# Performance work log

Hardware: AMD Instinct MI355X
Metric: run time of the kernel (lower is better)

## Reference

```python
import math
import jax, jax.numpy as jnp
import numpy as np

B, S, D, H = 2, 2048, 1024, 16


def setup_inputs() -> dict:
    key = jax.random.key(0)
    ks = jax.random.split(key, 8)
    scale = 1.0 / math.sqrt(D)
    kv_mask = jax.random.randint(ks[1], (B, S), 0, 2).astype(bool)
    kv_mask = kv_mask.at[:, 0].set(True)  # ensure at least one valid kv per batch
    return {
        "q": jax.random.normal(ks[0], (B, S, D), dtype=jnp.float32),
        "kv_mask": kv_mask,
        "Wq": jax.random.normal(ks[2], (D, D), dtype=jnp.float32) * scale,
        "Wk": jax.random.normal(ks[3], (D, D), dtype=jnp.float32) * scale,
        "Wv": jax.random.normal(ks[4], (D, D), dtype=jnp.float32) * scale,
        "Wo": jax.random.normal(ks[5], (D, D), dtype=jnp.float32) * scale,
        "bo": jax.random.normal(ks[6], (D,), dtype=jnp.float32) * 0.01,
        "num_heads": H,
    }


def _pass_with_mask(x, W, mask, b=None):
    # Linear applied everywhere, output zeroed where mask is False (pass_with_mask)
    y = x @ W.T
    if b is not None:
        y = y + b
    return jnp.where(mask[..., None], y, 0.0)


def reference(q, kv_mask, Wq, Wk, Wv, Wo, bo, num_heads):
    b, s, d = q.shape
    hd = d // num_heads
    q_mask = jnp.ones((b, s), dtype=bool)  # default q_mask in the module
    # self-attention: k = v = q
    qh = _pass_with_mask(q, Wq, q_mask).reshape(b, s, num_heads, hd)
    kh = _pass_with_mask(q, Wk, kv_mask).reshape(b, s, num_heads, hd)
    vh = _pass_with_mask(q, Wv, kv_mask).reshape(b, s, num_heads, hd)
    # scores: note the module scales by sqrt(model_dim), NOT sqrt(head_dim)
    scores = jnp.einsum("bqhd,bkhd->bhqk", qh, kh) / math.sqrt(d)
    mask = (q_mask[:, :, None] & kv_mask[:, None, :])[:, None, :, :]  # [b,1,q,k]
    scores = jnp.where(mask, scores, -jnp.inf)
    attn = jax.nn.softmax(scores, axis=-1)
    attn = jnp.where(mask, attn, 0.0)
    out = jnp.einsum("bhqk,bkhd->bqhd", attn, vh).reshape(b, s, d)
    return _pass_with_mask(out, Wo, q_mask, bo)
```

## Files before the change

kernel.cpp:

```cpp
#include <hip/hip_runtime.h>
#include <math.h>

#define B_ 2
#define S_ 2048
#define DM 1024
#define NH 16
#define HD 64

typedef unsigned short u16;
typedef unsigned int u32;
typedef __attribute__((ext_vector_type(8))) short bf16x8;
typedef __attribute__((ext_vector_type(4))) float f32x4;

#define C2SCALE 0.0450842200277800f

__device__ __forceinline__ u16 f2bf(float x) {
  unsigned u = __float_as_uint(x);
  u = (u + 0x7FFFu + ((u >> 16) & 1u)) >> 16;
  return (u16)u;
}

__device__ __forceinline__ u32 cvtpk(float lo, float hi) {
  u32 r;
  asm("v_cvt_pk_bf16_f32 %0, %1, %2" : "=v"(r) : "v"(lo), "v"(hi));
  return r;
}

__device__ __forceinline__ float exp2a(float x) {
  float r;
  asm("v_exp_f32 %0, %1" : "=v"(r) : "v"(x));
  return r;
}

__device__ __forceinline__ void gload_lds16(const u16* g, u16* l) {
  __builtin_amdgcn_global_load_lds((const __attribute__((address_space(1))) void*)g,
                                   (__attribute__((address_space(3))) void*)l, 16, 0, 0);
}

__device__ __forceinline__ int sigpos(int w6) {
  return ((w6 >> 5) << 5) | (((w6 >> 2) & 3) << 3) | (((w6 >> 4) & 1) << 2) | (w6 & 3);
}

__global__ void mask_scan(const int* __restrict__ kvm, int* __restrict__ posb,
                          int* __restrict__ nvb, u16* __restrict__ mwg) {
  const int b = blockIdx.x;
  const int tid = threadIdx.x;
  const int lane = tid & 63, wv = tid >> 6;
  __shared__ int wsum[4];
  int v[8], s = 0;
  const int base = b * S_ + tid * 8;
#pragma unroll
  for (int j = 0; j < 8; j++) { v[j] = kvm[base + j] ? 1 : 0; s += v[j]; }
  int sc = s;
#pragma unroll
  for (int off = 1; off < 64; off <<= 1) {
    int t = __shfl_up(sc, off, 64);
    if (lane >= off) sc += t;
  }
  if (lane == 63) wsum[wv] = sc;
  __syncthreads();
  int woff = 0;
#pragma unroll
  for (int w = 0; w < 4; w++) woff += (w < wv) ? wsum[w] : 0;
  int run = woff + sc - s;
#pragma unroll
  for (int j = 0; j < 8; j++) { posb[base + j] = run; run += v[j]; }
  const int total = wsum[0] + wsum[1] + wsum[2] + wsum[3];
  if (tid == 0) nvb[b] = total;
  for (int i = tid; i < S_; i += 256)
    mwg[b * S_ + (i & ~63) + sigpos(i & 63)] = (i < total) ? 0xFFFFu : 0u;
}

__global__ void cvt_all(const float* __restrict__ q, const float* __restrict__ Wq,
                        const float* __restrict__ Wk, const float* __restrict__ Wv,
                        const float* __restrict__ Wo, const int* __restrict__ kvm,
                        const int* __restrict__ posb, const int* __restrict__ nvb,
                        u16* __restrict__ Xbf, u16* __restrict__ Wcat,
                        u16* __restrict__ Wobf, u16* __restrict__ vtbuf,
                        u16* __restrict__ Xc) {
  const int NQ4 = (B_ * S_ * DM) / 4;
  const int NW4 = (DM * DM) / 4;
  const int total = NQ4 + 4 * NW4;
  int i = blockIdx.x * blockDim.x + threadIdx.x;
  int stride = gridDim.x * blockDim.x;
  for (int idx = i; idx < B_ * NH * HD * 64; idx += stride) {
    int col = idx & 63;
    int dd = (idx >> 6) & 63;
    int bh = idx >> 12;
    int nv = nvb[bh >> 4];
    int padw = ((nv + 63) & ~63) - nv;
    if (col < padw)
      vtbuf[((size_t)bh * HD + dd) * S_ + nv + col] = 0;
  }
  for (; i < total; i += stride) {
    if (i < NQ4) {
      float4 v = ((const float4*)q)[i];
      ushort4 o;
      o.x = f2bf(v.x); o.y = f2bf(v.y); o.z = f2bf(v.z); o.w = f2bf(v.w);
      ((ushort4*)Xbf)[i] = o;
      int row = i >> 8, chunk = i & 255;
      int b = row >> 11, s = row & 2047;
      if (kvm[b * S_ + s]) {
        int p = posb[b * S_ + s];
        *(ushort4*)(Xc + ((size_t)(b * S_ + p)) * DM + chunk * 4) = o;
      }
    } else {
      int t = i - NQ4;
      const float* src;
      u16* dst;
      if (t < NW4)            { src = Wq + (size_t)t * 4; dst = Wcat + (size_t)t * 4; }
      else if (t < 2 * NW4)   { src = Wk + (size_t)(t - NW4) * 4;     dst = Wcat + DM * DM + (size_t)(t - NW4) * 4; }
      else if (t < 3 * NW4)   { src = Wv + (size_t)(t - 2 * NW4) * 4; dst = Wcat + 2 * DM * DM + (size_t)(t - 2 * NW4) * 4; }
      else                    { src = Wo + (size_t)(t - 3 * NW4) * 4; dst = Wobf + (size_t)(t - 3 * NW4) * 4; }
      float4 v = *(const float4*)src;
      ushort4 o;
      o.x = f2bf(v.x); o.y = f2bf(v.y); o.z = f2bf(v.z); o.w = f2bf(v.w);
      *(ushort4*)dst = o;
    }
  }
}

__global__ __launch_bounds__(512, 6) void gemm_qkv(
    const u16* __restrict__ Xbf, const u16* __restrict__ Xc,
    const u16* __restrict__ Wcat, u16* __restrict__ qo, u16* __restrict__ ko,
    u16* __restrict__ vo, const int* __restrict__ nvb) {
  const int K = DM;
  const int Lraw = blockIdx.x;
  const int Ls = (Lraw & 7) * 96 + (Lraw >> 3);

  int Mb, nglob, bkv = 0, nv = 1 << 30;
  const u16* Ap;
  if (Ls < 256) {
    Mb = (Ls & 31) << 7;
    nglob = (Ls >> 5) << 7;
    Ap = Xbf;
  } else {
    int L2 = Ls - 256;
    bkv = L2 >> 8;
    int L3 = L2 & 255;
    Mb = (L3 & 15) << 7;
    nglob = 1024 + ((L3 >> 4) << 7);
    nv = nvb[bkv];
    if (Mb >= nv) return;
    Ap = Xc + (size_t)bkv * S_ * DM;
  }

  __shared__ __align__(16) u16 As[2][64 * 64];
  __shared__ __align__(16) u16 Bs[2][64 * 64];
  const int tid = threadIdx.x;
  const int wv = tid >> 6, lane = tid & 63;
  const int g = lane >> 4, c = lane & 15;
  const int wr = wv >> 1, wc = wv & 1;

  f32x4 acc[2][4];
#pragma unroll
  for (int i = 0; i < 2; i++)
#pragma unroll
    for (int j = 0; j < 4; j++) acc[i][j] = f32x4{0.f, 0.f, 0.f, 0.f};

  const int srow = tid >> 3;
  const int scol8 = tid & 7;
  const int m1 = srow * 2 + (scol8 >> 2);
  const int kkc = (scol8 & 3) * 8;
  const u16* ag = Ap + (size_t)(Mb + m1) * K + kkc;
  const u16* bg = Wcat + (size_t)(nglob + m1) * K + kkc;
  const int slot = scol8 ^ (srow & 7);
  u16* al = &As[0][srow * 64 + slot * 8];
  u16* bl = &Bs[0][srow * 64 + slot * 8];

  bf16x8 ar = *(const bf16x8*)ag;
  bf16x8 br = *(const bf16x8*)bg;
  *(bf16x8*)al = ar;
  *(bf16x8*)bl = br;
  ar = *(const bf16x8*)(ag + 32);
  br = *(const bf16x8*)(bg + 32);
  __syncthreads();

  const int off = ((((c & 1) << 2) | g) ^ (c >> 1)) << 3;
  const int arb = (wr * 16 + (c >> 1)) * 64 + off;
  const int brb = (wc * 32 + (c >> 1)) * 64 + off;

  for (int t = 0; t < 32; ++t) {
    const int cur = t & 1;
    if (t + 1 < 32) {
      const int nb = (cur ^ 1) * 4096;
      *(bf16x8*)(al + nb) = ar;
      *(bf16x8*)(bl + nb) = br;
      if (t + 2 < 32) {
        ar = *(const bf16x8*)(ag + (t + 2) * 32);
        br = *(const bf16x8*)(bg + (t + 2) * 32);
      }
    }
    const u16* AB = &As[cur][0];
    const u16* BB = &Bs[cur][0];
    bf16x8 af[2], bfr[4];
#pragma unroll
    for (int mi = 0; mi < 2; mi++)
      af[mi] = *(const bf16x8*)&AB[arb + mi * 512];
#pragma unroll
    for (int ni = 0; ni < 4; ni++)
      bfr[ni] = *(const bf16x8*)&BB[brb + ni * 512];
#pragma unroll
    for (int mi = 0; mi < 2; mi++)
#pragma unroll
      for (int ni = 0; ni < 4; ni++)
        acc[mi][ni] = __builtin_amdgcn_mfma_f32_16x16x32_bf16(af[mi], bfr[ni], acc[mi][ni], 0, 0, 0);
    asm volatile("s_waitcnt lgkmcnt(0)\n\ts_barrier" ::: "memory");
  }

  const int nbase = nglob + wc * 64 + c;
  const int which = nbase >> 10;
  if (which == 0) {
#pragma unroll
    for (int mi = 0; mi < 2; mi++) {
#pragma unroll
      for (int ni = 0; ni < 4; ni++) {
        int nn = nbase + ni * 16;
        int h = nn >> 6, d = nn & 63;
#pragma unroll
        for (int r = 0; r < 4; r++) {
          int row = Mb + wr * 32 + mi * 16 + g * 4 + r;
          int b0 = row >> 11, s0 = row & 2047;
          qo[(((size_t)(b0 * NH + h)) * S_ + s0) * HD + d] =
              f2bf(acc[mi][ni][r] * C2SCALE);
        }
      }
    }
  } else if (which == 1) {
#pragma unroll
    for (int mi = 0; mi < 2; mi++) {
#pragma unroll
      for (int r = 0; r < 4; r++) {
        int p = Mb + wr * 32 + mi * 16 + g * 4 + r;
        if (p < nv) {
#pragma unroll
          for (int ni = 0; ni < 4; ni++) {
            int nn = (nbase + ni * 16) & 1023;
            ko[((size_t)(bkv * NH + (nn >> 6)) * S_ + p) * HD + (nn & 63)] =
                f2bf(acc[mi][ni][r]);
          }
        }
      }
    }
  } else {
#pragma unroll
    for (int mi = 0; mi < 2; mi++) {
#pragma unroll
      for (int r = 0; r < 4; r++) {
        int p = Mb + wr * 32 + mi * 16 + g * 4 + r;
        if (p < nv) {
          int dst = (p & ~63) + sigpos(p & 63);
#pragma unroll
          for (int ni = 0; ni < 4; ni++) {
            int nn = (nbase + ni * 16) & 1023;
            vo[((size_t)((bkv * NH + (nn >> 6)) * HD + (nn & 63))) * S_ + dst] =
                f2bf(acc[mi][ni][r]);
          }
        }
      }
    }
  }
}

__global__ __launch_bounds__(256, 4) void gemm_n64(
    const u16* __restrict__ A, const u16* __restrict__ Bw,
    const float* __restrict__ bias, float* __restrict__ fo) {
  __shared__ __align__(16) u16 As[128 * 32];
  __shared__ __align__(16) u16 Bs[64 * 32];
  const int K = DM, N = DM;
  const int tid = threadIdx.x;
  const int wv = tid >> 6, lane = tid & 63;
  const int g = lane >> 4, c = lane & 15;
  const int wr = wv >> 1, wc = wv & 1;
  const int L = blockIdx.x;
  const int Ls = (L & 7) * 64 + (L >> 3);
  const int Mb = (Ls & 31) << 7, Nb = (Ls >> 5) << 6;

  f32x4 acc[4][2];
#pragma unroll
  for (int i = 0; i < 4; i++)
#pragma unroll
    for (int j = 0; j < 2; j++) acc[i][j] = f32x4{0.f, 0.f, 0.f, 0.f};

  for (int kb = 0; kb < K; kb += 32) {
#pragma unroll
    for (int it = 0; it < 2; ++it) {
      int id = it * 256 + tid;
      int m = id >> 2, kk = (id & 3) * 8;
      gload_lds16(A + (size_t)(Mb + m) * K + kb + kk, As + (it * 4 + wv) * 512);
    }
    {
      int m = tid >> 2, kk = (tid & 3) * 8;
      gload_lds16(Bw + (size_t)(Nb + m) * K + kb + kk, Bs + wv * 512);
    }
    __syncthreads();
    bf16x8 af[4], bfr[2];
#pragma unroll
    for (int mi = 0; mi < 4; mi++)
      af[mi] = *(const bf16x8*)(As + (wr * 64 + mi * 16 + c) * 32 + g * 8);
#pragma unroll
    for (int ni = 0; ni < 2; ni++)
      bfr[ni] = *(const bf16x8*)(Bs + (wc * 32 + ni * 16 + c) * 32 + g * 8);
#pragma unroll
    for (int mi = 0; mi < 4; mi++)
#pragma unroll
      for (int ni = 0; ni < 2; ni++)
        acc[mi][ni] = __builtin_amdgcn_mfma_f32_16x16x32_bf16(af[mi], bfr[ni], acc[mi][ni], 0, 0, 0);
    __syncthreads();
  }

#pragma unroll
  for (int mi = 0; mi < 4; mi++) {
#pragma unroll
    for (int ni = 0; ni < 2; ni++) {
      int n = Nb + wc * 32 + ni * 16 + c;
      float bv = bias[n];
#pragma unroll
      for (int r = 0; r < 4; r++) {
        int row = Mb + wr * 64 + mi * 16 + g * 4 + r;
        fo[(size_t)row * N + n] = acc[mi][ni][r] + bv;
      }
    }
  }
}

__global__ __launch_bounds__(512, 4) void attn_kernel(
    const u16* __restrict__ qb, const u16* __restrict__ kb,
    const u16* __restrict__ vtb, const u16* __restrict__ mwg,
    const int* __restrict__ nvb, u16* __restrict__ ob) {
  __shared__ __align__(16) u16 Kl[2][64 * 64];
  __shared__ __align__(16) u16 Vl[2][64 * 64];
  __shared__ __align__(16) u16 MW[S_];

  const int tid = threadIdx.x;
  const int wv = tid >> 6, lane = tid & 63;
  const int g = lane >> 4, c = lane & 15;

  const int L = blockIdx.x;
  const int j = L >> 3;
  const int bh = ((L & 7) << 2) | (j >> 4);
  const int qi = j & 15;
  const int b = bh >> 4, h = bh & 15;
  const int q0 = qi * 128;
  const size_t bhbase = (size_t)bh * (S_ * HD);
  const int NT = (nvb[b] + 63) >> 6;

  ((uint2*)MW)[tid] = ((const uint2*)(mwg + b * S_))[tid];

  bf16x8 qf[2];
#pragma unroll
  for (int ks = 0; ks < 2; ks++)
    qf[ks] = *(const bf16x8*)(qb + bhbase + (size_t)(q0 + wv * 16 + c) * HD + ks * 32 + g * 8);

  f32x4 Oa[4];
#pragma unroll
  for (int di = 0; di < 4; di++) Oa[di] = f32x4{0.f, 0.f, 0.f, 0.f};
  f32x4 lacc = f32x4{0.f, 0.f, 0.f, 0.f};

  union { u32 u[4]; bf16x8 v; } ones;
#pragma unroll
  for (int w = 0; w < 4; w++) ones.u[w] = 0x3F803F80u;

  const int srow = tid >> 3;
  const int scol8 = tid & 7;
  const u16* kg = kb + bhbase + (size_t)srow * HD + scol8 * 8;
  const u16* vg = vtb + bhbase + (size_t)srow * S_ + scol8 * 8;
  const int wslot = scol8 ^ (srow & 7);
  u16* kld = &Kl[0][srow * 64 + wslot * 8];
  u16* vld = &Vl[0][srow * 64 + wslot * 8];

  bf16x8 krg = *(const bf16x8*)kg;
  bf16x8 vrg = *(const bf16x8*)vg;
  *(bf16x8*)kld = krg;
  *(bf16x8*)vld = vrg;
  krg = *(const bf16x8*)(kg + 64 * HD);
  vrg = *(const bf16x8*)(vg + 64);
  __syncthreads();

  const int swz = c & 7;

  for (int t = 0; t < NT; ++t) {
    const int cur = t & 1;
    if (t + 1 < NT) {
      *(bf16x8*)(kld + (cur ^ 1) * 4096) = krg;
      *(bf16x8*)(vld + (cur ^ 1) * 4096) = vrg;
      if (t + 2 < NT) {
        krg = *(const bf16x8*)(kg + (t + 2) * (64 * HD));
        vrg = *(const bf16x8*)(vg + (t + 2) * 64);
      }
    }
    const u16* KB = &Kl[cur][0];
    const u16* VB = &Vl[cur][0];

    f32x4 Sa[4];
#pragma unroll
    for (int ni = 0; ni < 4; ni++) Sa[ni] = f32x4{0.f, 0.f, 0.f, 0.f};
    __builtin_amdgcn_s_setprio(1);
#pragma unroll
    for (int ks = 0; ks < 2; ks++) {
      bf16x8 kf[4];
#pragma unroll
      for (int ni = 0; ni < 4; ni++)
        kf[ni] = *(const bf16x8*)&KB[(ni * 16 + c) * 64 + (((4 * ks + g) ^ swz) * 8)];
#pragma unroll
      for (int ni = 0; ni < 4; ni++)
        Sa[ni] = __builtin_amdgcn_mfma_f32_16x16x32_bf16(kf[ni], qf[ks], Sa[ni], 0, 0, 0);
    }
    __builtin_amdgcn_s_setprio(0);

    bf16x8 Pa[2];
#pragma unroll
    for (int ks = 0; ks < 2; ks++) {
      uint4 mw = *(const uint4*)&MW[t * 64 + ks * 32 + g * 8];
      union { u32 u[4]; bf16x8 v; } pw;
      pw.u[0] = cvtpk(exp2a(Sa[2 * ks][0]), exp2a(Sa[2 * ks][1])) & mw.x;
      pw.u[1] = cvtpk(exp2a(Sa[2 * ks][2]), exp2a(Sa[2 * ks][3])) & mw.y;
      pw.u[2] = cvtpk(exp2a(Sa[2 * ks + 1][0]), exp2a(Sa[2 * ks + 1][1])) & mw.z;
      pw.u[3] = cvtpk(exp2a(Sa[2 * ks + 1][2]), exp2a(Sa[2 * ks + 1][3])) & mw.w;
      Pa[ks] = pw.v;
    }

    __builtin_amdgcn_s_setprio(1);
    lacc = __builtin_amdgcn_mfma_f32_16x16x32_bf16(ones.v, Pa[0], lacc, 0, 0, 0);
    lacc = __builtin_amdgcn_mfma_f32_16x16x32_bf16(ones.v, Pa[1], lacc, 0, 0, 0);
#pragma unroll
    for (int ks = 0; ks < 2; ks++) {
      bf16x8 vf[4];
#pragma unroll
      for (int di = 0; di < 4; di++)
        vf[di] = *(const bf16x8*)&VB[(di * 16 + c) * 64 + (((4 * ks + g) ^ swz) * 8)];
#pragma unroll
      for (int di = 0; di < 4; di++)
        Oa[di] = __builtin_amdgcn_mfma_f32_16x16x32_bf16(vf[di], Pa[ks], Oa[di], 0, 0, 0);
    }
    __builtin_amdgcn_s_setprio(0);

    asm volatile("s_waitcnt lgkmcnt(0)\n\ts_barrier" ::: "memory");
  }

  float inv = 1.f / lacc[0];
  int q = q0 + wv * 16 + c;
  size_t base = ((size_t)(b * S_ + q)) * DM + (size_t)h * HD;
#pragma unroll
  for (int di = 0; di < 4; di++) {
    uint2 o;
    o.x = cvtpk(Oa[di][0] * inv, Oa[di][1] * inv);
    o.y = cvtpk(Oa[di][2] * inv, Oa[di][3] * inv);
    *(uint2*)(ob + base + di * 16 + g * 4) = o;
  }
}

extern "C" void kernel_launch(void* const* d_in, const int* in_sizes, int n_in,
                              void* d_out, int out_size, void* d_ws, size_t ws_size,
                              hipStream_t stream) {
  const float* q  = (const float*)d_in[0];
  const int* kvm  = (const int*)d_in[1];
  const float* Wq = (const float*)d_in[2];
  const float* Wk = (const float*)d_in[3];
  const float* Wv = (const float*)d_in[4];
  const float* Wo = (const float*)d_in[5];
  const float* bo = (const float*)d_in[6];
  float* out = (float*)d_out;
  char* ws = (char*)d_ws;

  u16* Xbf   = (u16*)(ws);
  u16* Wcat  = (u16*)(ws + (8u << 20));
  u16* Wobf  = (u16*)(ws + (14u << 20));
  u16* qbuf  = (u16*)(ws + (16u << 20));
  u16* kbuf  = (u16*)(ws + (24u << 20));
  u16* vtbuf = (u16*)(ws + (32u << 20));
  u16* mwg   = (u16*)(ws + (40u << 20));
  int* posb  = (int*)(ws + (41u << 20));
  int* nvb   = (int*)(ws + (42u << 20));
  u16* Xc    = (u16*)d_out;
  u16* obuf  = Xbf;

  mask_scan<<<B_, 256, 0, stream>>>(kvm, posb, nvb, mwg);
  cvt_all<<<2048, 256, 0, stream>>>(q, Wq, Wk, Wv, Wo, kvm, posb, nvb,
                                    Xbf, Wcat, Wobf, vtbuf, Xc);
  gemm_qkv<<<768, 512, 0, stream>>>(Xbf, Xc, Wcat, qbuf, kbuf, vtbuf, nvb);
  attn_kernel<<<512, 512, 0, stream>>>(qbuf, kbuf, vtbuf, mwg, nvb, obuf);
  gemm_n64<<<512, 256, 0, stream>>>(obuf, Wobf, bo, out);
}
```

Before: 110.3 us.

## Give each attention wave two 16-row query tiles and halve the block size

The attention kernel now launches 256 threads per block (4 waves), and each wave handles 32 query rows as two 16-row MFMA tiles instead of 16 rows. Every K/V fragment read from shared memory feeds two MFMAs, which halves LDS traffic per unit of compute. Each thread now loads two K/V staging chunks per tile. The cost is roughly double the accumulator and fragment registers per thread, with launch bounds lowered to 256 threads and 3 blocks per CU. That means fewer waves per CU to hide latency.

```diff
diff --git a/kernel.cpp b/kernel.cpp
--- a/kernel.cpp
+++ b/kernel.cpp
@@ -324,7 +324,7 @@
   }
 }
 
-__global__ __launch_bounds__(512, 4) void attn_kernel(
+__global__ __launch_bounds__(256, 3) void attn_kernel(
     const u16* __restrict__ qb, const u16* __restrict__ kb,
     const u16* __restrict__ vtb, const u16* __restrict__ mwg,
     const int* __restrict__ nvb, u16* __restrict__ ob) {
@@ -345,17 +345,24 @@
   const size_t bhbase = (size_t)bh * (S_ * HD);
   const int NT = (nvb[b] + 63) >> 6;
 
-  ((uint2*)MW)[tid] = ((const uint2*)(mwg + b * S_))[tid];
-
-  bf16x8 qf[2];
-#pragma unroll
-  for (int ks = 0; ks < 2; ks++)
-    qf[ks] = *(const bf16x8*)(qb + bhbase + (size_t)(q0 + wv * 16 + c) * HD + ks * 32 + g * 8);
-
-  f32x4 Oa[4];
-#pragma unroll
-  for (int di = 0; di < 4; di++) Oa[di] = f32x4{0.f, 0.f, 0.f, 0.f};
-  f32x4 lacc = f32x4{0.f, 0.f, 0.f, 0.f};
+  ((uint4*)MW)[tid] = ((const uint4*)(mwg + b * S_))[tid];
+
+  bf16x8 qf[2][2];
+#pragma unroll
+  for (int mi = 0; mi < 2; mi++)
+#pragma unroll
+    for (int ks = 0; ks < 2; ks++)
+      qf[mi][ks] = *(const bf16x8*)(qb + bhbase +
+                   (size_t)(q0 + wv * 32 + mi * 16 + c) * HD + ks * 32 + g * 8);
+
+  f32x4 Oa[4][2];
+#pragma unroll
+  for (int di = 0; di < 4; di++)
+#pragma unroll
+    for (int mi = 0; mi < 2; mi++) Oa[di][mi] = f32x4{0.f, 0.f, 0.f, 0.f};
+  f32x4 lacc[2];
+  lacc[0] = f32x4{0.f, 0.f, 0.f, 0.f};
+  lacc[1] = f32x4{0.f, 0.f, 0.f, 0.f};
 
   union { u32 u[4]; bf16x8 v; } ones;
 #pragma unroll
@@ -363,18 +370,23 @@
 
   const int srow = tid >> 3;
   const int scol8 = tid & 7;
-  const u16* kg = kb + bhbase + (size_t)srow * HD + scol8 * 8;
-  const u16* vg = vtb + bhbase + (size_t)srow * S_ + scol8 * 8;
+  const u16* kg1 = kb + bhbase + (size_t)srow * HD + scol8 * 8;
+  const u16* kg2 = kg1 + (size_t)32 * HD;
+  const u16* vg1 = vtb + bhbase + (size_t)srow * S_ + scol8 * 8;
+  const u16* vg2 = vg1 + (size_t)32 * S_;
   const int wslot = scol8 ^ (srow & 7);
-  u16* kld = &Kl[0][srow * 64 + wslot * 8];
-  u16* vld = &Vl[0][srow * 64 + wslot * 8];
-
-  bf16x8 krg = *(const bf16x8*)kg;
-  bf16x8 vrg = *(const bf16x8*)vg;
-  *(bf16x8*)kld = krg;
-  *(bf16x8*)vld = vrg;
-  krg = *(const bf16x8*)(kg + 64 * HD);
-  vrg = *(const bf16x8*)(vg + 64);
+  u16* kld1 = &Kl[0][srow * 64 + wslot * 8];
+  u16* kld2 = kld1 + 32 * 64;
+  u16* vld1 = &Vl[0][srow * 64 + wslot * 8];
+  u16* vld2 = vld1 + 32 * 64;
+
+  bf16x8 krg[2], vrg[2];
+  krg[0] = *(const bf16x8*)kg1;  krg[1] = *(const bf16x8*)kg2;
+  vrg[0] = *(const bf16x8*)vg1;  vrg[1] = *(const bf16x8*)vg2;
+  *(bf16x8*)kld1 = krg[0];  *(bf16x8*)kld2 = krg[1];
+  *(bf16x8*)vld1 = vrg[0];  *(bf16x8*)vld2 = vrg[1];
+  krg[0] = *(const bf16x8*)(kg1 + 4096);  krg[1] = *(const bf16x8*)(kg2 + 4096);
+  vrg[0] = *(const bf16x8*)(vg1 + 64);    vrg[1] = *(const bf16x8*)(vg2 + 64);
   __syncthreads();
 
   const int swz = c & 7;
@@ -382,19 +394,24 @@
   for (int t = 0; t < NT; ++t) {
     const int cur = t & 1;
     if (t + 1 < NT) {
-      *(bf16x8*)(kld + (cur ^ 1) * 4096) = krg;
-      *(bf16x8*)(vld + (cur ^ 1) * 4096) = vrg;
+      const int nb = (cur ^ 1) * 4096;
+      *(bf16x8*)(kld1 + nb) = krg[0];  *(bf16x8*)(kld2 + nb) = krg[1];
+      *(bf16x8*)(vld1 + nb) = vrg[0];  *(bf16x8*)(vld2 + nb) = vrg[1];
       if (t + 2 < NT) {
-        krg = *(const bf16x8*)(kg + (t + 2) * (64 * HD));
-        vrg = *(const bf16x8*)(vg + (t + 2) * 64);
+        krg[0] = *(const bf16x8*)(kg1 + (t + 2) * 4096);
+        krg[1] = *(const bf16x8*)(kg2 + (t + 2) * 4096);
+        vrg[0] = *(const bf16x8*)(vg1 + (t + 2) * 64);
+        vrg[1] = *(const bf16x8*)(vg2 + (t + 2) * 64);
       }
     }
     const u16* KB = &Kl[cur][0];
     const u16* VB = &Vl[cur][0];
 
-    f32x4 Sa[4];
-#pragma unroll
-    for (int ni = 0; ni < 4; ni++) Sa[ni] = f32x4{0.f, 0.f, 0.f, 0.f};
+    f32x4 Sa[4][2];
+#pragma unroll
+    for (int ni = 0; ni < 4; ni++)
+#pragma unroll
+      for (int mi = 0; mi < 2; mi++) Sa[ni][mi] = f32x4{0.f, 0.f, 0.f, 0.f};
     __builtin_amdgcn_s_setprio(1);
 #pragma unroll
     for (int ks = 0; ks < 2; ks++) {
@@ -404,25 +421,33 @@
         kf[ni] = *(const bf16x8*)&KB[(ni * 16 + c) * 64 + (((4 * ks + g) ^ swz) * 8)];
 #pragma unroll
       for (int ni = 0; ni < 4; ni++)
-        Sa[ni] = __builtin_amdgcn_mfma_f32_16x16x32_bf16(kf[ni], qf[ks], Sa[ni], 0, 0, 0);
+#pragma unroll
+        for (int mi = 0; mi < 2; mi++)
+          Sa[ni][mi] = __builtin_amdgcn_mfma_f32_16x16x32_bf16(kf[ni], qf[mi][ks], Sa[ni][mi], 0, 0, 0);
     }
     __builtin_amdgcn_s_setprio(0);
 
-    bf16x8 Pa[2];
+    bf16x8 Pa[2][2];
 #pragma unroll
     for (int ks = 0; ks < 2; ks++) {
       uint4 mw = *(const uint4*)&MW[t * 64 + ks * 32 + g * 8];
-      union { u32 u[4]; bf16x8 v; } pw;
-      pw.u[0] = cvtpk(exp2a(Sa[2 * ks][0]), exp2a(Sa[2 * ks][1])) & mw.x;
-      pw.u[1] = cvtpk(exp2a(Sa[2 * ks][2]), exp2a(Sa[2 * ks][3])) & mw.y;
-      pw.u[2] = cvtpk(exp2a(Sa[2 * ks + 1][0]), exp2a(Sa[2 * ks + 1][1])) & mw.z;
-      pw.u[3] = cvtpk(exp2a(Sa[2 * ks + 1][2]), exp2a(Sa[2 * ks + 1][3])) & mw.w;
-      Pa[ks] = pw.v;
+#pragma unroll
+      for (int mi = 0; mi < 2; mi++) {
+        union { u32 u[4]; bf16x8 v; } pw;
+        pw.u[0] = cvtpk(exp2a(Sa[2 * ks][mi][0]), exp2a(Sa[2 * ks][mi][1])) & mw.x;
+        pw.u[1] = cvtpk(exp2a(Sa[2 * ks][mi][2]), exp2a(Sa[2 * ks][mi][3])) & mw.y;
+        pw.u[2] = cvtpk(exp2a(Sa[2 * ks + 1][mi][0]), exp2a(Sa[2 * ks + 1][mi][1])) & mw.z;
+        pw.u[3] = cvtpk(exp2a(Sa[2 * ks + 1][mi][2]), exp2a(Sa[2 * ks + 1][mi][3])) & mw.w;
+        Pa[mi][ks] = pw.v;
+      }
     }
 
     __builtin_amdgcn_s_setprio(1);
-    lacc = __builtin_amdgcn_mfma_f32_16x16x32_bf16(ones.v, Pa[0], lacc, 0, 0, 0);
-    lacc = __builtin_amdgcn_mfma_f32_16x16x32_bf16(ones.v, Pa[1], lacc, 0, 0, 0);
+#pragma unroll
+    for (int mi = 0; mi < 2; mi++) {
+      lacc[mi] = __builtin_amdgcn_mfma_f32_16x16x32_bf16(ones.v, Pa[mi][0], lacc[mi], 0, 0, 0);
+      lacc[mi] = __builtin_amdgcn_mfma_f32_16x16x32_bf16(ones.v, Pa[mi][1], lacc[mi], 0, 0, 0);
+    }
 #pragma unroll
     for (int ks = 0; ks < 2; ks++) {
       bf16x8 vf[4];
@@ -431,22 +456,27 @@
         vf[di] = *(const bf16x8*)&VB[(di * 16 + c) * 64 + (((4 * ks + g) ^ swz) * 8)];
 #pragma unroll
       for (int di = 0; di < 4; di++)
-        Oa[di] = __builtin_amdgcn_mfma_f32_16x16x32_bf16(vf[di], Pa[ks], Oa[di], 0, 0, 0);
+#pragma unroll
+        for (int mi = 0; mi < 2; mi++)
+          Oa[di][mi] = __builtin_amdgcn_mfma_f32_16x16x32_bf16(vf[di], Pa[mi][ks], Oa[di][mi], 0, 0, 0);
     }
     __builtin_amdgcn_s_setprio(0);
 
     asm volatile("s_waitcnt lgkmcnt(0)\n\ts_barrier" ::: "memory");
   }
 
-  float inv = 1.f / lacc[0];
-  int q = q0 + wv * 16 + c;
-  size_t base = ((size_t)(b * S_ + q)) * DM + (size_t)h * HD;
-#pragma unroll
-  for (int di = 0; di < 4; di++) {
-    uint2 o;
-    o.x = cvtpk(Oa[di][0] * inv, Oa[di][1] * inv);
-    o.y = cvtpk(Oa[di][2] * inv, Oa[di][3] * inv);
-    *(uint2*)(ob + base + di * 16 + g * 4) = o;
+#pragma unroll
+  for (int mi = 0; mi < 2; mi++) {
+    float inv = 1.f / lacc[mi][0];
+    int q = q0 + wv * 32 + mi * 16 + c;
+    size_t base = ((size_t)(b * S_ + q)) * DM + (size_t)h * HD;
+#pragma unroll
+    for (int di = 0; di < 4; di++) {
+      uint2 o;
+      o.x = cvtpk(Oa[di][mi][0] * inv, Oa[di][mi][1] * inv);
+      o.y = cvtpk(Oa[di][mi][2] * inv, Oa[di][mi][3] * inv);
+      *(uint2*)(ob + base + di * 16 + g * 4) = o;
+    }
   }
 }
 
@@ -479,6 +509,6 @@
   cvt_all<<<2048, 256, 0, stream>>>(q, Wq, Wk, Wv, Wo, kvm, posb, nvb,
                                     Xbf, Wcat, Wobf, vtbuf, Xc);
   gemm_qkv<<<768, 512, 0, stream>>>(Xbf, Xc, Wcat, qbuf, kbuf, vtbuf, nvb);
-  attn_kernel<<<512, 512, 0, stream>>>(qbuf, kbuf, vtbuf, mwg, nvb, obuf);
+  attn_kernel<<<512, 256, 0, stream>>>(qbuf, kbuf, vtbuf, mwg, nvb, obuf);
   gemm_n64<<<512, 256, 0, stream>>>(obuf, Wobf, bo, out);
 }
```

Result: no change. 111.2 us (+0.8%).
